# Kernel optimization log

Hardware: AMD Instinct MI355X
Metric: run time of the kernel (lower is better)

The kernel has to match this reference:

```python
import jax, jax.numpy as jnp
import numpy as np

COMMITMENT_COST = 0.25


def setup_inputs() -> dict:
    key = jax.random.key(0)
    k1, k2 = jax.random.split(key)
    B, D, H, W = 64, 64, 32, 32
    K = 512
    x = jax.random.normal(k1, (B, D, H, W), dtype=jnp.float32)
    # torch init: uniform_(-1/K, 1/K)
    codebook = jax.random.uniform(k2, (K, D), dtype=jnp.float32,
                                  minval=-1.0 / K, maxval=1.0 / K)
    return {"x": x, "codebook": codebook}


def reference(x, codebook):
    B, D, H, W = x.shape
    K = codebook.shape[0]
    in_re = jnp.transpose(x, (0, 2, 3, 1))          # [B,H,W,D]
    flat = in_re.reshape(-1, D)                      # [N,D], N=B*H*W
    dist = (jnp.sum(flat * flat, axis=1, keepdims=True)
            + jnp.sum(codebook * codebook, axis=1)
            - 2.0 * jnp.matmul(flat, codebook.T))    # [N,K]
    idx = jnp.argmin(dist, axis=1)                   # [N]
    encoding = jax.nn.one_hot(idx, K, dtype=jnp.float32)  # [N,K]
    softmax_histogram = jnp.sum(jax.nn.softmax(-dist, axis=-1).reshape(B, -1, K), axis=1)  # [B,K]
    quantized = jnp.matmul(encoding, codebook).reshape(in_re.shape)  # [B,H,W,D]
    e_latent_loss = jnp.mean((jax.lax.stop_gradient(quantized) - in_re) ** 2)
    q_latent_loss = jnp.mean((quantized - jax.lax.stop_gradient(in_re)) ** 2)
    loss = q_latent_loss + COMMITMENT_COST * e_latent_loss
    # straight-through estimator
    quant_st = in_re + jax.lax.stop_gradient(quantized - in_re)
    avg_probs = jnp.mean(encoding, axis=0)
    perplexity = jnp.exp(-jnp.sum(avg_probs * jnp.log(avg_probs + 1e-10)))
    quant_out = jnp.transpose(quant_st, (0, 3, 1, 2))  # back to NCHW
    encoding_indice = idx.reshape(B, -1)               # [B, H*W]
    # per-batch histogram of code usage == sum of one-hots over spatial dim
    index_program = jnp.sum(encoding.reshape(B, -1, K), axis=1)  # [B,K]
    return (quant_out, loss, perplexity, encoding_indice, index_program, softmax_histogram)
```

## Files before the change

kernel.cpp:

```cpp
#include <hip/hip_runtime.h>


#define OFF_LOSS 4194304
#define OFF_PERP 4194305
#define OFF_ENC  4194306
#define OFF_IP   4259842
#define OFF_SH   4292610

#define WS_CBT   0
#define WS_CE2   32768
#define WS_SHP   33280
#define WS_LOSS  557568


typedef float f16v __attribute__((ext_vector_type(16)));

typedef __attribute__((address_space(1))) const void g_void;
typedef __attribute__((address_space(3))) void lds_void;
#define GLOAD_LDS(G, S) \
    __builtin_amdgcn_global_load_lds((g_void*)(G), (lds_void*)(S), 16, 0, 0)

__global__ __launch_bounds__(256) void vq_prep(const float* __restrict__ cb,
                                               float* __restrict__ ws)
{
    const int t  = blockIdx.x * 256 + threadIdx.x;
    const int kg = t >> 4;
    const int j  = t & 15;
    const float4 v = ((const float4*)cb)[(kg << 4) + j];
    float pr = v.x * v.x + v.y * v.y + v.z * v.z + v.w * v.w;
    #pragma unroll
    for (int off = 1; off < 16; off <<= 1) pr += __shfl_xor(pr, off, 16);
    if (j == 0) ws[WS_CE2 + kg] = pr;
    const int kc = kg >> 7, kl = kg & 127;
    float* base = ws + WS_CBT + (kc << 13) + (j << 9) + kl;
    base[0]   = v.x;
    base[128] = v.y;
    base[256] = v.z;
    base[384] = v.w;
}

#define FMA4(ACC, AV, K4) \
    ACC[(K4) + 0] = fmaf((AV), bq.x, ACC[(K4) + 0]); \
    ACC[(K4) + 1] = fmaf((AV), bq.y, ACC[(K4) + 1]); \
    ACC[(K4) + 2] = fmaf((AV), bq.z, ACC[(K4) + 2]); \
    ACC[(K4) + 3] = fmaf((AV), bq.w, ACC[(K4) + 3]);

#define STAGE_CST(KC) do { \
    GLOAD_LDS(&cbT4[((KC) << 11) + t],        &csT4[t]); \
    GLOAD_LDS(&cbT4[((KC) << 11) + 256 + t],  &csT4[256 + t]); \
    GLOAD_LDS(&cbT4[((KC) << 11) + 512 + t],  &csT4[512 + t]); \
    GLOAD_LDS(&cbT4[((KC) << 11) + 768 + t],  &csT4[768 + t]); \
    GLOAD_LDS(&cbT4[((KC) << 11) + 1024 + t], &csT4[1024 + t]); \
    GLOAD_LDS(&cbT4[((KC) << 11) + 1280 + t], &csT4[1280 + t]); \
    GLOAD_LDS(&cbT4[((KC) << 11) + 1536 + t], &csT4[1536 + t]); \
    GLOAD_LDS(&cbT4[((KC) << 11) + 1792 + t], &csT4[1792 + t]); \
} while (0)

#define GEMM_COMPUTE(KC) do { \
    _Pragma("unroll 2") \
    for (int db = 0; db < 16; ++db) { \
        const float* cbase = &csT[(db << 9) + (tc << 2)]; \
        _Pragma("unroll") \
        for (int j = 0; j < 4; ++j) { \
            const int d = (db << 2) + j; \
            const float4 a0 = *(const float4*)&xs[(d << 6) + (tr << 3)]; \
            const float4 a1 = *(const float4*)&xs[(d << 6) + (tr << 3) + 4]; \
            const float4 bq = *(const float4*)&cbase[j << 7]; \
            FMA4(acc0, a0.x, (KC) << 2) \
            FMA4(acc1, a0.y, (KC) << 2) \
            FMA4(acc2, a0.z, (KC) << 2) \
            FMA4(acc3, a0.w, (KC) << 2) \
            FMA4(acc4, a1.x, (KC) << 2) \
            FMA4(acc5, a1.y, (KC) << 2) \
            FMA4(acc6, a1.z, (KC) << 2) \
            FMA4(acc7, a1.w, (KC) << 2) \
        } \
    } \
} while (0)

#define EPI_C(C, ACC) { \
    const int k = (((C) >> 2) << 7) + (tc << 2) + ((C) & 3); \
    const float t1 = xxr + ce2[k]; \
    const float dist = t1 - 2.f * ACC[C]; \
    ACC[C] = dist; \
    if (dist < m) { m = dist; bk = k; } }

#define EXP_C(C, ACC) { \
    const float e = __expf(m - ACC[C]); \
    ACC[C] = e; z += e; }

#define ROW_EPI(I, ACC, INVZ) do { \
    const int row = (tr << 3) + (I); \
    const float xxr = sxx[row]; \
    float m = 1e30f; int bk = 0; \
    EPI_C(0, ACC)  EPI_C(1, ACC)  EPI_C(2, ACC)  EPI_C(3, ACC) \
    EPI_C(4, ACC)  EPI_C(5, ACC)  EPI_C(6, ACC)  EPI_C(7, ACC) \
    EPI_C(8, ACC)  EPI_C(9, ACC)  EPI_C(10, ACC) EPI_C(11, ACC) \
    EPI_C(12, ACC) EPI_C(13, ACC) EPI_C(14, ACC) EPI_C(15, ACC) \
    _Pragma("unroll") \
    for (int off = 1; off < 32; off <<= 1) { \
        const float mo = __shfl_xor(m, off, 32); \
        const int   ko = __shfl_xor(bk, off, 32); \
        if (mo < m || (mo == m && ko < bk)) { m = mo; bk = ko; } \
    } \
    float z = 0.f; \
    EXP_C(0, ACC)  EXP_C(1, ACC)  EXP_C(2, ACC)  EXP_C(3, ACC) \
    EXP_C(4, ACC)  EXP_C(5, ACC)  EXP_C(6, ACC)  EXP_C(7, ACC) \
    EXP_C(8, ACC)  EXP_C(9, ACC)  EXP_C(10, ACC) EXP_C(11, ACC) \
    EXP_C(12, ACC) EXP_C(13, ACC) EXP_C(14, ACC) EXP_C(15, ACC) \
    _Pragma("unroll") \
    for (int off = 1; off < 32; off <<= 1) z += __shfl_xor(z, off, 32); \
    INVZ = 1.f / z; \
    if (tc == 0) { \
        sidx[row] = bk; \
        enc[((size_t)b << 10) + row0 + row] = (float)bk; \
    } \
} while (0)

#define HIST_C(C) { \
    const int k = (((C) >> 2) << 7) + (tc << 2) + ((C) & 3); \
    float cs = 0.f; \
    cs += acc0[C] * invz0; cs += acc1[C] * invz1; \
    cs += acc2[C] * invz2; cs += acc3[C] * invz3; \
    cs += acc4[C] * invz4; cs += acc5[C] * invz5; \
    cs += acc6[C] * invz6; cs += acc7[C] * invz7; \
    atomicAdd(&shist[k], cs); }

__global__ __launch_bounds__(256, 1) void vq_main(
    const float* __restrict__ x, const float* __restrict__ cb,
    const float* __restrict__ wsc,
    float* __restrict__ wso,
    float* __restrict__ out)
{
    __shared__ float  xs[64 * 64];
    __shared__ float  csT[64 * 128];
    __shared__ float  ce2[512];
    __shared__ float  sxx[64];
    __shared__ int    sidx[64];

    const int t    = threadIdx.x;
    const int blk  = blockIdx.x;
    const int b    = blk >> 4;
    const int row0 = (blk & 15) << 6;
    const int tr   = t >> 5;
    const int tc   = t & 31;

    const float4* cbT4 = (const float4*)(wsc + WS_CBT);
    float4* csT4 = (float4*)csT;

    {
        const float4* xb4 = (const float4*)(x + ((size_t)b << 16) + row0);
        #pragma unroll
        for (int p = 0; p < 4; ++p) {
            const int fi = (p << 8) + t;
            const int d  = fi >> 4;
            const int r4 = fi & 15;
            GLOAD_LDS(&xb4[(d << 8) + r4], &xs[(d << 6) + (r4 << 2)]);
        }
    }
    STAGE_CST(0);
    if (t < 128) ((float4*)ce2)[t] = ((const float4*)(wsc + WS_CE2))[t];

    __syncthreads();

    if (t < 64) {
        float s = 0.f;
        for (int d = 0; d < 64; ++d) { const float v = xs[(d << 6) + t]; s = fmaf(v, v, s); }
        sxx[t] = s;
    }

    f16v acc0 = 0.f, acc1 = 0.f, acc2 = 0.f, acc3 = 0.f;
    f16v acc4 = 0.f, acc5 = 0.f, acc6 = 0.f, acc7 = 0.f;

    GEMM_COMPUTE(0);
    __syncthreads();
    STAGE_CST(1);
    __syncthreads();
    GEMM_COMPUTE(1);
    __syncthreads();
    STAGE_CST(2);
    __syncthreads();
    GEMM_COMPUTE(2);
    __syncthreads();
    STAGE_CST(3);
    __syncthreads();
    GEMM_COMPUTE(3);

    float* enc = out + OFF_ENC;
    float invz0, invz1, invz2, invz3, invz4, invz5, invz6, invz7;
    ROW_EPI(0, acc0, invz0);
    ROW_EPI(1, acc1, invz1);
    ROW_EPI(2, acc2, invz2);
    ROW_EPI(3, acc3, invz3);
    ROW_EPI(4, acc4, invz4);
    ROW_EPI(5, acc5, invz5);
    ROW_EPI(6, acc6, invz6);
    ROW_EPI(7, acc7, invz7);

    __syncthreads();

    float* shist = csT;
    shist[t] = 0.f; shist[t + 256] = 0.f;
    __syncthreads();
    HIST_C(0)  HIST_C(1)  HIST_C(2)  HIST_C(3)
    HIST_C(4)  HIST_C(5)  HIST_C(6)  HIST_C(7)
    HIST_C(8)  HIST_C(9)  HIST_C(10) HIST_C(11)
    HIST_C(12) HIST_C(13) HIST_C(14) HIST_C(15)
    __syncthreads();
    {
        float* wsh = wso + WS_SHP + ((size_t)blk << 9);
        wsh[t]       = shist[t];
        wsh[t + 256] = shist[t + 256];
    }

    const int r4 = (t & 15) << 2;
    const int dq = t >> 4;
    const int c0 = sidx[r4], c1 = sidx[r4 + 1], c2 = sidx[r4 + 2], c3 = sidx[r4 + 3];
    float lsum = 0.f;
    #pragma unroll
    for (int p = 0; p < 4; ++p) {
        const int d = (p << 4) + dq;
        float4 q;
        q.x = cb[(c0 << 6) + d];
        q.y = cb[(c1 << 6) + d];
        q.z = cb[(c2 << 6) + d];
        q.w = cb[(c3 << 6) + d];
        const float4 xv = *(const float4*)&xs[(d << 6) + r4];
        const float d0 = q.x - xv.x, d1 = q.y - xv.y, d2 = q.z - xv.z, d3 = q.w - xv.w;
        lsum = fmaf(d0, d0, lsum); lsum = fmaf(d1, d1, lsum);
        lsum = fmaf(d2, d2, lsum); lsum = fmaf(d3, d3, lsum);
        *(float4*)&out[(((size_t)(b << 6) + d) << 10) + row0 + r4] = q;
    }
    #pragma unroll
    for (int off = 1; off < 64; off <<= 1) lsum += __shfl_xor(lsum, off, 64);
    if ((t & 63) == 0) wso[WS_LOSS + (blk << 2) + (t >> 6)] = lsum;
}

__global__ __launch_bounds__(512) void vq_reduce(const float* __restrict__ ws,
                                                 float* __restrict__ out)
{
    __shared__ int hist[512];
    const int b = blockIdx.x, t = threadIdx.x;
    const float* p = ws + WS_SHP + ((size_t)b << 13) + t;
    float s = 0.f;
    #pragma unroll
    for (int j = 0; j < 16; ++j) s += p[j << 9];
    out[OFF_SH + (b << 9) + t] = s;
    hist[t] = 0;
    __syncthreads();
    const float* enc = out + OFF_ENC + ((size_t)b << 10);
    const int ca = (int)enc[t];
    const int cbn = (int)enc[t + 512];
    atomicAdd(&hist[ca], 1);
    atomicAdd(&hist[cbn], 1);
    __syncthreads();
    out[OFF_IP + (b << 9) + t] = (float)hist[t];
}

__global__ __launch_bounds__(512) void vq_final(const float* __restrict__ ws,
                                                float* __restrict__ out)
{
    __shared__ float red[8], red2[8];
    const int t = threadIdx.x;
    const float* ip = out + OFF_IP;
    float c0 = 0.f, c1 = 0.f, c2 = 0.f, c3 = 0.f;
    #pragma unroll
    for (int bb = 0; bb < 64; bb += 4) {
        c0 += ip[((bb + 0) << 9) + t];
        c1 += ip[((bb + 1) << 9) + t];
        c2 += ip[((bb + 2) << 9) + t];
        c3 += ip[((bb + 3) << 9) + t];
    }
    const float c = (c0 + c1) + (c2 + c3);
    const float pav = c * (1.0f / 65536.f);
    float h = pav * logf(pav + 1e-10f);
    const float* wl = ws + WS_LOSS;
    float ls = 0.f;
    #pragma unroll
    for (int j = 0; j < 8; ++j) ls += wl[(j << 9) + t];
    #pragma unroll
    for (int off = 1; off < 64; off <<= 1) {
        h  += __shfl_xor(h, off, 64);
        ls += __shfl_xor(ls, off, 64);
    }
    if ((t & 63) == 0) { red[t >> 6] = h; red2[t >> 6] = ls; }
    __syncthreads();
    if (t == 0) {
        float H = 0.f, L = 0.f;
        #pragma unroll
        for (int w = 0; w < 8; ++w) { H += red[w]; L += red2[w]; }
        out[OFF_PERP] = expf(-H);
        out[OFF_LOSS] = L * (1.25f / 4194304.f);
    }
}

extern "C" void kernel_launch(void* const* d_in, const int* in_sizes, int n_in,
                              void* d_out, int out_size, void* d_ws, size_t ws_size,
                              hipStream_t stream)
{
    const float* x  = (const float*)d_in[0];
    const float* cb = (const float*)d_in[1];
    float* out = (float*)d_out;
    float* ws  = (float*)d_ws;
    (void)ws_size;

    vq_prep  <<<32,   256, 0, stream>>>(cb, ws);
    vq_main  <<<1024, 256, 0, stream>>>(x, cb, ws, ws, out);
    vq_reduce<<<64,   512, 0, stream>>>(ws, out);
    vq_final <<<1,    512, 0, stream>>>(ws, out);
}
```

Before: 172.9 us.

## Stage full transposed codebook in LDS once and fuse GEMM loop over all chunks

Loads the whole 128KB transposed codebook into LDS in one burst instead of four 32KB chunks separated by barriers. The GEMM becomes a single d-loop that reads the x operands once per d and updates all four K-chunks, removing the serialized stage/sync pairs and the repeated xs loads. LDS use grows to about 150KB per block, which stays within MI355X LDS and matches the one-block-per-CU launch bound. All loads are now issued before the first barrier, so the first compute waits for the full transfer.

Result: slower. 189.3 us (+9.5%).

```diff
diff --git a/kernel.cpp b/kernel.cpp
--- a/kernel.cpp
+++ b/kernel.cpp
@@ -45,37 +45,16 @@
     ACC[(K4) + 2] = fmaf((AV), bq.z, ACC[(K4) + 2]); \
     ACC[(K4) + 3] = fmaf((AV), bq.w, ACC[(K4) + 3]);
 
-#define STAGE_CST(KC) do { \
-    GLOAD_LDS(&cbT4[((KC) << 11) + t],        &csT4[t]); \
-    GLOAD_LDS(&cbT4[((KC) << 11) + 256 + t],  &csT4[256 + t]); \
-    GLOAD_LDS(&cbT4[((KC) << 11) + 512 + t],  &csT4[512 + t]); \
-    GLOAD_LDS(&cbT4[((KC) << 11) + 768 + t],  &csT4[768 + t]); \
-    GLOAD_LDS(&cbT4[((KC) << 11) + 1024 + t], &csT4[1024 + t]); \
-    GLOAD_LDS(&cbT4[((KC) << 11) + 1280 + t], &csT4[1280 + t]); \
-    GLOAD_LDS(&cbT4[((KC) << 11) + 1536 + t], &csT4[1536 + t]); \
-    GLOAD_LDS(&cbT4[((KC) << 11) + 1792 + t], &csT4[1792 + t]); \
-} while (0)
-
-#define GEMM_COMPUTE(KC) do { \
-    _Pragma("unroll 2") \
-    for (int db = 0; db < 16; ++db) { \
-        const float* cbase = &csT[(db << 9) + (tc << 2)]; \
-        _Pragma("unroll") \
-        for (int j = 0; j < 4; ++j) { \
-            const int d = (db << 2) + j; \
-            const float4 a0 = *(const float4*)&xs[(d << 6) + (tr << 3)]; \
-            const float4 a1 = *(const float4*)&xs[(d << 6) + (tr << 3) + 4]; \
-            const float4 bq = *(const float4*)&cbase[j << 7]; \
-            FMA4(acc0, a0.x, (KC) << 2) \
-            FMA4(acc1, a0.y, (KC) << 2) \
-            FMA4(acc2, a0.z, (KC) << 2) \
-            FMA4(acc3, a0.w, (KC) << 2) \
-            FMA4(acc4, a1.x, (KC) << 2) \
-            FMA4(acc5, a1.y, (KC) << 2) \
-            FMA4(acc6, a1.z, (KC) << 2) \
-            FMA4(acc7, a1.w, (KC) << 2) \
-        } \
-    } \
+#define FMA_CHUNK(KC) do { \
+    const float4 bq = *(const float4*)&csT[((KC) << 13) + (d << 7) + (tc << 2)]; \
+    FMA4(acc0, a0.x, (KC) << 2) \
+    FMA4(acc1, a0.y, (KC) << 2) \
+    FMA4(acc2, a0.z, (KC) << 2) \
+    FMA4(acc3, a0.w, (KC) << 2) \
+    FMA4(acc4, a1.x, (KC) << 2) \
+    FMA4(acc5, a1.y, (KC) << 2) \
+    FMA4(acc6, a1.z, (KC) << 2) \
+    FMA4(acc7, a1.w, (KC) << 2) \
 } while (0)
 
 #define EPI_C(C, ACC) { \
@@ -132,8 +111,8 @@
     float* __restrict__ wso,
     float* __restrict__ out)
 {
+    __shared__ float  csT[4 * 64 * 128];
     __shared__ float  xs[64 * 64];
-    __shared__ float  csT[64 * 128];
     __shared__ float  ce2[512];
     __shared__ float  sxx[64];
     __shared__ int    sidx[64];
@@ -157,8 +136,10 @@
             const int r4 = fi & 15;
             GLOAD_LDS(&xb4[(d << 8) + r4], &xs[(d << 6) + (r4 << 2)]);
         }
-    }
-    STAGE_CST(0);
+        #pragma unroll
+        for (int q = 0; q < 32; ++q)
+            GLOAD_LDS(&cbT4[(q << 8) + t], &csT4[(q << 8) + t]);
+    }
     if (t < 128) ((float4*)ce2)[t] = ((const float4*)(wsc + WS_CE2))[t];
 
     __syncthreads();
@@ -172,19 +153,17 @@
     f16v acc0 = 0.f, acc1 = 0.f, acc2 = 0.f, acc3 = 0.f;
     f16v acc4 = 0.f, acc5 = 0.f, acc6 = 0.f, acc7 = 0.f;
 
-    GEMM_COMPUTE(0);
-    __syncthreads();
-    STAGE_CST(1);
-    __syncthreads();
-    GEMM_COMPUTE(1);
-    __syncthreads();
-    STAGE_CST(2);
-    __syncthreads();
-    GEMM_COMPUTE(2);
-    __syncthreads();
-    STAGE_CST(3);
-    __syncthreads();
-    GEMM_COMPUTE(3);
+    #pragma unroll 4
+    for (int d = 0; d < 64; ++d) {
+        const float4 a0 = *(const float4*)&xs[(d << 6) + (tr << 3)];
+        const float4 a1 = *(const float4*)&xs[(d << 6) + (tr << 3) + 4];
+        FMA_CHUNK(0);
+        FMA_CHUNK(1);
+        FMA_CHUNK(2);
+        FMA_CHUNK(3);
+    }
+
+    __syncthreads();
 
     float* enc = out + OFF_ENC;
     float invz0, invz1, invz2, invz3, invz4, invz5, invz6, invz7;
```

## Fuse reduce and final kernels into main via last-block atomic counters

Applied to the files above, without the earlier changes.

Removes the separate vq_reduce and vq_final launches. Each vq_main block bumps a per-batch counter after a threadfence, and the last of the 16 blocks for a batch does that batch's softmax-histogram and index histogram reduction. A global counter then picks the last batch block to compute perplexity and loss. This saves two kernel launches and their gaps, at the cost of extra atomics and fences at the tail of every block.

New measurement: 263.6 us. +52.5%, slower.

```diff
diff --git a/kernel.cpp b/kernel.cpp
--- a/kernel.cpp
+++ b/kernel.cpp
@@ -11,6 +11,7 @@
 #define WS_CE2   32768
 #define WS_SHP   33280
 #define WS_LOSS  557568
+#define WS_CNT   561664
 
 
 typedef float f16v __attribute__((ext_vector_type(16)));
@@ -23,6 +24,9 @@
 __global__ __launch_bounds__(256) void vq_prep(const float* __restrict__ cb,
                                                float* __restrict__ ws)
 {
+    if (blockIdx.x == 0 && threadIdx.x < 65)
+        ((int*)ws)[WS_CNT + threadIdx.x] = 0;
+
     const int t  = blockIdx.x * 256 + threadIdx.x;
     const int kg = t >> 4;
     const int j  = t & 15;
@@ -137,6 +141,7 @@
     __shared__ float  ce2[512];
     __shared__ float  sxx[64];
     __shared__ int    sidx[64];
+    __shared__ int    s_last;
 
     const int t    = threadIdx.x;
     const int blk  = blockIdx.x;
@@ -234,63 +239,99 @@
     #pragma unroll
     for (int off = 1; off < 64; off <<= 1) lsum += __shfl_xor(lsum, off, 64);
     if ((t & 63) == 0) wso[WS_LOSS + (blk << 2) + (t >> 6)] = lsum;
-}
-
-__global__ __launch_bounds__(512) void vq_reduce(const float* __restrict__ ws,
-                                                 float* __restrict__ out)
-{
-    __shared__ int hist[512];
-    const int b = blockIdx.x, t = threadIdx.x;
-    const float* p = ws + WS_SHP + ((size_t)b << 13) + t;
-    float s = 0.f;
-    #pragma unroll
-    for (int j = 0; j < 16; ++j) s += p[j << 9];
-    out[OFF_SH + (b << 9) + t] = s;
-    hist[t] = 0;
-    __syncthreads();
-    const float* enc = out + OFF_ENC + ((size_t)b << 10);
-    const int ca = (int)enc[t];
-    const int cbn = (int)enc[t + 512];
-    atomicAdd(&hist[ca], 1);
-    atomicAdd(&hist[cbn], 1);
-    __syncthreads();
-    out[OFF_IP + (b << 9) + t] = (float)hist[t];
-}
-
-__global__ __launch_bounds__(512) void vq_final(const float* __restrict__ ws,
-                                                float* __restrict__ out)
-{
-    __shared__ float red[8], red2[8];
-    const int t = threadIdx.x;
-    const float* ip = out + OFF_IP;
-    float c0 = 0.f, c1 = 0.f, c2 = 0.f, c3 = 0.f;
-    #pragma unroll
-    for (int bb = 0; bb < 64; bb += 4) {
-        c0 += ip[((bb + 0) << 9) + t];
-        c1 += ip[((bb + 1) << 9) + t];
-        c2 += ip[((bb + 2) << 9) + t];
-        c3 += ip[((bb + 3) << 9) + t];
-    }
-    const float c = (c0 + c1) + (c2 + c3);
-    const float pav = c * (1.0f / 65536.f);
-    float h = pav * logf(pav + 1e-10f);
-    const float* wl = ws + WS_LOSS;
-    float ls = 0.f;
-    #pragma unroll
-    for (int j = 0; j < 8; ++j) ls += wl[(j << 9) + t];
-    #pragma unroll
-    for (int off = 1; off < 64; off <<= 1) {
-        h  += __shfl_xor(h, off, 64);
-        ls += __shfl_xor(ls, off, 64);
-    }
-    if ((t & 63) == 0) { red[t >> 6] = h; red2[t >> 6] = ls; }
-    __syncthreads();
-    if (t == 0) {
-        float H = 0.f, L = 0.f;
+
+    int* cnts = (int*)wso;
+    __threadfence();
+    if (t == 0) s_last = (atomicAdd(&cnts[WS_CNT + b], 1) == 15);
+    __syncthreads();
+    if (!s_last) return;
+
+    {
+        const float* p = wso + WS_SHP + (((size_t)b << 4) << 9);
+        float s0 = 0.f, s1 = 0.f;
         #pragma unroll
-        for (int w = 0; w < 8; ++w) { H += red[w]; L += red2[w]; }
-        out[OFF_PERP] = expf(-H);
-        out[OFF_LOSS] = L * (1.25f / 4194304.f);
+        for (int j = 0; j < 16; ++j) {
+            s0 += p[(j << 9) + t];
+            s1 += p[(j << 9) + t + 256];
+        }
+        out[OFF_SH + (b << 9) + t]       = s0;
+        out[OFF_SH + (b << 9) + t + 256] = s1;
+    }
+    {
+        int* hist = (int*)csT;
+        hist[t] = 0; hist[t + 256] = 0;
+        __syncthreads();
+        const float* encb = out + OFF_ENC + ((size_t)b << 10);
+        atomicAdd(&hist[(int)encb[t]], 1);
+        atomicAdd(&hist[(int)encb[t + 256]], 1);
+        atomicAdd(&hist[(int)encb[t + 512]], 1);
+        atomicAdd(&hist[(int)encb[t + 768]], 1);
+        __syncthreads();
+        out[OFF_IP + (b << 9) + t]       = (float)hist[t];
+        out[OFF_IP + (b << 9) + t + 256] = (float)hist[t + 256];
+    }
+
+    __threadfence();
+    if (t == 0) s_last = (atomicAdd(&cnts[WS_CNT + 64], 1) == 63);
+    __syncthreads();
+    if (!s_last) return;
+
+    {
+        float ha, hb;
+        {
+            float c0 = 0.f, c1 = 0.f, c2 = 0.f, c3 = 0.f;
+            #pragma unroll
+            for (int bb = 0; bb < 64; bb += 4) {
+                c0 += out[OFF_IP + ((bb + 0) << 9) + t];
+                c1 += out[OFF_IP + ((bb + 1) << 9) + t];
+                c2 += out[OFF_IP + ((bb + 2) << 9) + t];
+                c3 += out[OFF_IP + ((bb + 3) << 9) + t];
+            }
+            const float c = (c0 + c1) + (c2 + c3);
+            const float pav = c * (1.0f / 65536.f);
+            ha = pav * logf(pav + 1e-10f);
+        }
+        {
+            float c0 = 0.f, c1 = 0.f, c2 = 0.f, c3 = 0.f;
+            #pragma unroll
+            for (int bb = 0; bb < 64; bb += 4) {
+                c0 += out[OFF_IP + ((bb + 0) << 9) + t + 256];
+                c1 += out[OFF_IP + ((bb + 1) << 9) + t + 256];
+                c2 += out[OFF_IP + ((bb + 2) << 9) + t + 256];
+                c3 += out[OFF_IP + ((bb + 3) << 9) + t + 256];
+            }
+            const float c = (c0 + c1) + (c2 + c3);
+            const float pav = c * (1.0f / 65536.f);
+            hb = pav * logf(pav + 1e-10f);
+        }
+        float la = 0.f, lb = 0.f;
+        #pragma unroll
+        for (int j = 0; j < 8; ++j) {
+            la += wso[WS_LOSS + (j << 9) + t];
+            lb += wso[WS_LOSS + (j << 9) + t + 256];
+        }
+        #pragma unroll
+        for (int off = 1; off < 64; off <<= 1) {
+            ha += __shfl_xor(ha, off, 64);
+            hb += __shfl_xor(hb, off, 64);
+            la += __shfl_xor(la, off, 64);
+            lb += __shfl_xor(lb, off, 64);
+        }
+        __shared__ float sra[4], srb[4], s2a[4], s2b[4];
+        if ((t & 63) == 0) {
+            const int w = t >> 6;
+            sra[w] = ha; srb[w] = hb; s2a[w] = la; s2b[w] = lb;
+        }
+        __syncthreads();
+        if (t == 0) {
+            float H = 0.f, L = 0.f;
+            H += sra[0]; H += sra[1]; H += sra[2]; H += sra[3];
+            H += srb[0]; H += srb[1]; H += srb[2]; H += srb[3];
+            L += s2a[0]; L += s2a[1]; L += s2a[2]; L += s2a[3];
+            L += s2b[0]; L += s2b[1]; L += s2b[2]; L += s2b[3];
+            out[OFF_PERP] = expf(-H);
+            out[OFF_LOSS] = L * (1.25f / 4194304.f);
+        }
     }
 }
 
@@ -304,8 +345,6 @@
     float* ws  = (float*)d_ws;
     (void)ws_size;
 
-    vq_prep  <<<32,   256, 0, stream>>>(cb, ws);
-    vq_main  <<<1024, 256, 0, stream>>>(x, cb, ws, ws, out);
-    vq_reduce<<<64,   512, 0, stream>>>(ws, out);
-    vq_final <<<1,    512, 0, stream>>>(ws, out);
+    vq_prep <<<32,   256, 0, stream>>>(cb, ws);
+    vq_main <<<1024, 256, 0, stream>>>(x, cb, ws, ws, out);
 }
```
